# Performance work log

Measured on AMD Instinct MI355X. Metric: run time of the kernel, lower is better.

The kernel has to match this reference:

```python
import jax, jax.numpy as jnp
import numpy as np

N = 100000      # nodes
E = 1600000     # edges (avg degree 16)
IN = 128        # in_channels
HID = 32        # hidden_channels per head
HEADS = 4
OUT = 64        # out_channels
NEG_SLOPE = 0.2 # PyG GATConv default leaky_relu slope


def setup_inputs() -> dict:
    key = jax.random.key(0)
    ks = jax.random.split(key, 12)
    def glorot(k, shape):
        fan = shape[0] + shape[-1]
        s = jnp.sqrt(6.0 / fan)
        return jax.random.uniform(k, shape, jnp.float32, -s, s)
    return {
        "x": jax.random.normal(ks[0], (N, IN), jnp.float32),
        "edge_index": jax.random.randint(ks[1], (2, E), 0, N, dtype=jnp.int64),
        # GATConv layer 1: in=IN, out=HID per head, heads=HEADS, concat=True
        "W1": glorot(ks[2], (IN, HEADS * HID)),
        "a_src1": glorot(ks[3], (HEADS, HID)),
        "a_dst1": glorot(ks[4], (HEADS, HID)),
        "b1": jnp.zeros((HEADS * HID,), jnp.float32),
        # GATConv layer 2: in=HEADS*HID, out=OUT, heads=1, concat=False
        "W2": glorot(ks[5], (HEADS * HID, OUT)),
        "a_src2": glorot(ks[6], (1, OUT)),
        "a_dst2": glorot(ks[7], (1, OUT)),
        "b2": jnp.zeros((OUT,), jnp.float32),
    }


def _gat_layer(x, src, dst, W, a_src, a_dst, bias, num_nodes, concat):
    """PyG-style GATConv (add_self_loops already applied to src/dst).
    x: [N, F_in]; src/dst: [E']; W: [F_in, H*C]; a_*: [H, C]."""
    H, C = a_src.shape
    h = (x @ W).reshape(-1, H, C)                       # [N, H, C]
    # per-node attention scores (avoid gathering full features for logits)
    e_src = (h * a_src[None]).sum(-1)                   # [N, H]
    e_dst = (h * a_dst[None]).sum(-1)                   # [N, H]
    logits = jax.nn.leaky_relu(e_src[src] + e_dst[dst], NEG_SLOPE)  # [E', H]
    # segment softmax over incoming edges of each destination node
    mx = jax.ops.segment_max(logits, dst, num_segments=num_nodes)   # [N, H]
    ex = jnp.exp(logits - mx[dst])                      # [E', H]
    den = jax.ops.segment_sum(ex, dst, num_segments=num_nodes)      # [N, H]
    alpha = ex / (den[dst] + 1e-16)                     # [E', H]
    # weighted message aggregation
    msg = h[src] * alpha[..., None]                     # [E', H, C]
    out = jax.ops.segment_sum(msg, dst, num_segments=num_nodes)     # [N, H, C]
    if concat:
        out = out.reshape(num_nodes, H * C)
    else:
        out = out.mean(axis=1)
    return out + bias


def reference(x, edge_index, W1, a_src1, a_dst1, b1, W2, a_src2, a_dst2, b2):
    n = x.shape[0]
    loops = jnp.arange(n, dtype=edge_index.dtype)
    src = jnp.concatenate([edge_index[0], loops])       # add self-loops (PyG default)
    dst = jnp.concatenate([edge_index[1], loops])
    # dropout layers are identity in eval mode
    h = _gat_layer(x, src, dst, W1, a_src1, a_dst1, b1, n, concat=True)
    h = jax.nn.elu(h)
    out = _gat_layer(h, src, dst, W2, a_src2, a_dst2, b2, n, concat=False)
    return out
```

## Files before the change

### kernel.cpp

```cpp
#include <hip/hip_runtime.h>
#include <cmath>

#define IN_F 128
#define NEG_SLOPE 0.2f
#define SEG 64
#define BSHIFT 7
#define NBMAX 1024
#define CHUNK 2048
#define SLOT 4096
#define LDSTRIDE 136

typedef short bfrag8 __attribute__((ext_vector_type(8)));
typedef float facc4 __attribute__((ext_vector_type(4)));

__device__ __forceinline__ int ldidx(const int* ei, int pos, int is64) {
  return is64 ? ei[2 * pos] : ei[pos];
}
__device__ __forceinline__ unsigned short f2b(float f) {
  unsigned u = __float_as_uint(f);
  u += 0x7fffu + ((u >> 16) & 1u);
  return (unsigned short)(u >> 16);
}
__device__ __forceinline__ float b2f_lo(unsigned u) { return __uint_as_float(u << 16); }
__device__ __forceinline__ float b2f_hi(unsigned u) { return __uint_as_float(u & 0xffff0000u); }
__device__ __forceinline__ float b2f_us(unsigned short us) { return __uint_as_float(((unsigned)us) << 16); }
__device__ __forceinline__ void wave_lds_fence() {
  asm volatile("s_waitcnt lgkmcnt(0)" ::: "memory");
}
__device__ __forceinline__ float leaky(float l) { return fmaxf(l, NEG_SLOPE * l); }

__global__ __launch_bounds__(256) void detect_kernel(const int* __restrict__ ei, int E, int* __restrict__ flag) {
  __shared__ int red[256];
  int acc = 0;
  int limit = E < 4096 ? E : 4096;
  for (int j = threadIdx.x; j < limit; j += 256) acc |= ei[2 * j + 1];
  red[threadIdx.x] = acc;
  __syncthreads();
  for (int s = 128; s > 0; s >>= 1) {
    if ((int)threadIdx.x < s) red[threadIdx.x] |= red[threadIdx.x + s];
    __syncthreads();
  }
  if (threadIdx.x == 0) *flag = (red[0] == 0) ? 1 : 0;
}

__global__ __launch_bounds__(1024) void binit_kernel(int* __restrict__ bcur, int NB) {
  int tid = threadIdx.x;
  if (tid < NB) bcur[tid] = tid * SLOT;
}

__global__ __launch_bounds__(256) void bscatter_kernel(const int* __restrict__ ei, int E, int Etot,
                                                       const int* __restrict__ flag, int NB,
                                                       int* __restrict__ bcur, unsigned* __restrict__ ebuf) {
  __shared__ int hcnt[NBMAX];
  __shared__ int hcur[NBMAX];
  int tid = threadIdx.x;
  int base = blockIdx.x * CHUNK;
  int cnt = Etot - base; if (cnt > CHUNK) cnt = CHUNK;
  int is64 = *flag;
  for (int i = tid; i < NB; i += 256) hcnt[i] = 0;
  __syncthreads();
  for (int i = tid; i < cnt; i += 256) {
    int e = base + i;
    int d = (e < E) ? ldidx(ei, E + e, is64) : (e - E);
    atomicAdd(&hcnt[d >> BSHIFT], 1);
  }
  __syncthreads();
  for (int i = tid; i < NB; i += 256) {
    int c = hcnt[i];
    hcur[i] = c ? atomicAdd(&bcur[i], c) : 0;
  }
  __syncthreads();
  for (int i = tid; i < cnt; i += 256) {
    int e = base + i;
    int s, d;
    if (e < E) { s = ldidx(ei, e, is64); d = ldidx(ei, E + e, is64); }
    else       { s = e - E; d = s; }
    int pos = atomicAdd(&hcur[d >> BSHIFT], 1);
    ebuf[pos] = ((unsigned)s << 7) | ((unsigned)d & 127u);
  }
}

__global__ __launch_bounds__(256) void bcsr_kernel(const int* __restrict__ bcur, const unsigned* __restrict__ ebuf,
                                                   int* __restrict__ rowptr, int* __restrict__ rowdeg,
                                                   int* __restrict__ csr, int N, int NB) {
  __shared__ int cnt[128];
  __shared__ int cur[128];
  __shared__ int w0sum;
  int tid = threadIdx.x;
  int b = blockIdx.x;
  int lo = b * SLOT, hi = bcur[b];
  int node0 = b << BSHIFT;
  int nn = N - node0; if (nn > 128) nn = 128;
  if (tid < 128) cnt[tid] = 0;
  __syncthreads();
  for (int i = lo + tid; i < hi; i += 256) {
    atomicAdd(&cnt[ebuf[i] & 127u], 1);
  }
  __syncthreads();
  int v = 0, incl = 0;
  if (tid < 128) {
    v = cnt[tid];
    incl = v;
    int lane = tid & 63;
    #pragma unroll
    for (int off = 1; off < 64; off <<= 1) { int t = __shfl_up(incl, off); if (lane >= off) incl += t; }
    if (tid == 63) w0sum = incl;
  }
  __syncthreads();
  if (tid < 128) {
    if (tid >= 64) incl += w0sum;
    int excl = incl - v;
    cur[tid] = excl;
    if (tid < nn) {
      rowptr[node0 + tid] = lo + excl;
      rowdeg[node0 + tid] = v;
    }
  }
  __syncthreads();
  for (int i = lo + tid; i < hi; i += 256) {
    unsigned pr = ebuf[i];
    int p = atomicAdd(&cur[pr & 127u], 1);
    csr[lo + p] = (int)(pr >> 7);
  }
}

__global__ __launch_bounds__(256) void gemm1_kernel(
    const float* __restrict__ x, const float* __restrict__ W,
    const float* __restrict__ asr, const float* __restrict__ ads,
    unsigned short* __restrict__ h1b, float* __restrict__ es, float* __restrict__ ed,
    int N) {
  __shared__ short Wt[128 * LDSTRIDE];
  __shared__ short As[64 * LDSTRIDE];
  int tid = threadIdx.x;
  int row0 = blockIdx.x * 64;
  int lane = tid & 63, wv = tid >> 6;
  int m2 = lane & 15, quad = lane >> 4;

  for (int i = tid; i < 128 * 128; i += 256) {
    int k = i >> 7, c = i & 127;
    Wt[c * LDSTRIDE + k] = (short)f2b(W[i]);
  }
  for (int idx = tid; idx < 64 * 16; idx += 256) {
    int r = idx >> 4, ch = idx & 15;
    int n = row0 + r;
    bfrag8 sv;
    if (n < N) {
      float4 v0 = *(const float4*)&x[(size_t)n * 128 + ch * 8];
      float4 v1 = *(const float4*)&x[(size_t)n * 128 + ch * 8 + 4];
      sv[0] = (short)f2b(v0.x); sv[1] = (short)f2b(v0.y);
      sv[2] = (short)f2b(v0.z); sv[3] = (short)f2b(v0.w);
      sv[4] = (short)f2b(v1.x); sv[5] = (short)f2b(v1.y);
      sv[6] = (short)f2b(v1.z); sv[7] = (short)f2b(v1.w);
    } else {
      sv = (bfrag8)0;
    }
    *(bfrag8*)&As[r * LDSTRIDE + ch * 8] = sv;
  }
  __syncthreads();

  facc4 acc[8] = {};
  const short* Abase = &As[(wv * 16 + m2) * LDSTRIDE];
  #pragma unroll
  for (int ks = 0; ks < 4; ++ks) {
    int k = ks * 32 + quad * 8;
    bfrag8 af = *(const bfrag8*)&Abase[k];
    #pragma unroll
    for (int t = 0; t < 8; ++t) {
      bfrag8 bf = *(const bfrag8*)&Wt[(t * 16 + m2) * LDSTRIDE + k];
      acc[t] = __builtin_amdgcn_mfma_f32_16x16x32_bf16(af, bf, acc[t], 0, 0, 0);
    }
  }

  float av[8], bv[8];
  #pragma unroll
  for (int t = 0; t < 8; ++t) {
    int ai = (t >> 1) * 32 + (t & 1) * 16 + m2;
    av[t] = asr[ai]; bv[t] = ads[ai];
  }
  #pragma unroll
  for (int r = 0; r < 4; ++r) {
    int n = row0 + wv * 16 + quad * 4 + r;
    bool valid = (n < N);
    if (valid) {
      #pragma unroll
      for (int t = 0; t < 8; ++t)
        h1b[(size_t)n * 128 + t * 16 + m2] = f2b(acc[t][r]);
    }
    #pragma unroll
    for (int h = 0; h < 4; ++h) {
      float ps = acc[2 * h][r] * av[2 * h] + acc[2 * h + 1][r] * av[2 * h + 1];
      float pd = acc[2 * h][r] * bv[2 * h] + acc[2 * h + 1][r] * bv[2 * h + 1];
      ps += __shfl_xor(ps, 1); ps += __shfl_xor(ps, 2); ps += __shfl_xor(ps, 4); ps += __shfl_xor(ps, 8);
      pd += __shfl_xor(pd, 1); pd += __shfl_xor(pd, 2); pd += __shfl_xor(pd, 4); pd += __shfl_xor(pd, 8);
      if (valid && m2 == 0) {
        es[(size_t)n * 4 + h] = ps;
        ed[(size_t)n * 4 + h] = pd;
      }
    }
  }
}

__global__ __launch_bounds__(256) void gemm2_kernel(
    const unsigned short* __restrict__ xb, const float* __restrict__ W,
    const float* __restrict__ asr, const float* __restrict__ ads,
    unsigned short* __restrict__ h2b, float* __restrict__ es, float* __restrict__ ed,
    int N) {
  __shared__ short Wt[64 * LDSTRIDE];
  __shared__ short As[64 * LDSTRIDE];
  int tid = threadIdx.x;
  int row0 = blockIdx.x * 64;
  int lane = tid & 63, wv = tid >> 6;
  int m2 = lane & 15, quad = lane >> 4;

  for (int i = tid; i < 128 * 64; i += 256) {
    int k = i >> 6, c = i & 63;
    Wt[c * LDSTRIDE + k] = (short)f2b(W[i]);
  }
  for (int idx = tid; idx < 64 * 16; idx += 256) {
    int r = idx >> 4, ch = idx & 15;
    int n = row0 + r;
    uint4 u = (n < N) ? *(const uint4*)&xb[(size_t)n * 128 + ch * 8]
                      : make_uint4(0, 0, 0, 0);
    *(uint4*)&As[r * LDSTRIDE + ch * 8] = u;
  }
  __syncthreads();

  facc4 acc[4] = {};
  const short* Abase = &As[(wv * 16 + m2) * LDSTRIDE];
  #pragma unroll
  for (int ks = 0; ks < 4; ++ks) {
    int k = ks * 32 + quad * 8;
    bfrag8 af = *(const bfrag8*)&Abase[k];
    #pragma unroll
    for (int t = 0; t < 4; ++t) {
      bfrag8 bf = *(const bfrag8*)&Wt[(t * 16 + m2) * LDSTRIDE + k];
      acc[t] = __builtin_amdgcn_mfma_f32_16x16x32_bf16(af, bf, acc[t], 0, 0, 0);
    }
  }

  float av[4], bv[4];
  #pragma unroll
  for (int t = 0; t < 4; ++t) {
    av[t] = asr[t * 16 + m2]; bv[t] = ads[t * 16 + m2];
  }
  #pragma unroll
  for (int r = 0; r < 4; ++r) {
    int n = row0 + wv * 16 + quad * 4 + r;
    bool valid = (n < N);
    if (valid) {
      #pragma unroll
      for (int t = 0; t < 4; ++t)
        h2b[(size_t)n * 64 + t * 16 + m2] = f2b(acc[t][r]);
    }
    float ps = acc[0][r] * av[0] + acc[1][r] * av[1] + acc[2][r] * av[2] + acc[3][r] * av[3];
    float pd = acc[0][r] * bv[0] + acc[1][r] * bv[1] + acc[2][r] * bv[2] + acc[3][r] * bv[3];
    ps += __shfl_xor(ps, 1); ps += __shfl_xor(ps, 2); ps += __shfl_xor(ps, 4); ps += __shfl_xor(ps, 8);
    pd += __shfl_xor(pd, 1); pd += __shfl_xor(pd, 2); pd += __shfl_xor(pd, 4); pd += __shfl_xor(pd, 8);
    if (valid && m2 == 0) { es[n] = ps; ed[n] = pd; }
  }
}

__global__ __launch_bounds__(256) void agg1_kernel(
    const int* __restrict__ rowptr, const int* __restrict__ rowdeg, const int* __restrict__ csr,
    const float* __restrict__ es, const float* __restrict__ ed,
    const unsigned short* __restrict__ h1b, const float* __restrict__ bias1,
    unsigned short* __restrict__ hmidb, int N) {
  __shared__ unsigned short lds_ab[4][4][SEG + 4][4];
  __shared__ int lds_s[4][4][SEG + 4];
  int tid = threadIdx.x;
  int wv = tid >> 6, lane = tid & 63;
  int sub = lane >> 4, sj = lane & 15;
  int nbase = blockIdx.x * 16 + wv * 4;
  int n = nbase + sub;
  bool nvalid = (n < N);
  int start = 0, len = 0;
  if (nvalid) { start = rowptr[n]; len = rowdeg[n]; }
  int lenc = (len <= SEG) ? len : 0;

  float4 edv = nvalid ? ((const float4*)ed)[n] : make_float4(0.f, 0.f, 0.f, 0.f);
  float l[4][4];
  float mx = -1e30f;
  #pragma unroll
  for (int it = 0; it < 4; ++it) {
    int j = sj + it * 16;
    if (j < lenc) {
      int s = csr[start + j];
      lds_s[wv][sub][j] = s;
      float4 ev = ((const float4*)es)[s];
      float l0 = leaky(ev.x + edv.x);
      float l1 = leaky(ev.y + edv.y);
      float l2 = leaky(ev.z + edv.z);
      float l3 = leaky(ev.w + edv.w);
      l[it][0] = l0; l[it][1] = l1; l[it][2] = l2; l[it][3] = l3;
      mx = fmaxf(mx, fmaxf(fmaxf(l0, l1), fmaxf(l2, l3)));
    } else {
      l[it][0] = -1e30f; l[it][1] = -1e30f; l[it][2] = -1e30f; l[it][3] = -1e30f;
    }
  }
  #pragma unroll
  for (int off = 1; off < 16; off <<= 1) mx = fmaxf(mx, __shfl_xor(mx, off));

  float s0 = 0.f, s1 = 0.f, s2 = 0.f, s3 = 0.f;
  #pragma unroll
  for (int it = 0; it < 4; ++it) {
    float p0 = __expf(l[it][0] - mx);
    float p1 = __expf(l[it][1] - mx);
    float p2 = __expf(l[it][2] - mx);
    float p3 = __expf(l[it][3] - mx);
    l[it][0] = p0; l[it][1] = p1; l[it][2] = p2; l[it][3] = p3;
    s0 += p0; s1 += p1; s2 += p2; s3 += p3;
  }
  #pragma unroll
  for (int off = 1; off < 16; off <<= 1) {
    s0 += __shfl_xor(s0, off); s1 += __shfl_xor(s1, off);
    s2 += __shfl_xor(s2, off); s3 += __shfl_xor(s3, off);
  }
  float i0 = __builtin_amdgcn_rcpf(s0 + 1e-16f);
  float i1 = __builtin_amdgcn_rcpf(s1 + 1e-16f);
  float i2 = __builtin_amdgcn_rcpf(s2 + 1e-16f);
  float i3 = __builtin_amdgcn_rcpf(s3 + 1e-16f);
  #pragma unroll
  for (int it = 0; it < 4; ++it) {
    int j = sj + it * 16;
    if (j < lenc) {
      unsigned pk0 = (unsigned)f2b(l[it][0] * i0) | ((unsigned)f2b(l[it][1] * i1) << 16);
      unsigned pk1 = (unsigned)f2b(l[it][2] * i2) | ((unsigned)f2b(l[it][3] * i3) << 16);
      *(unsigned*)&lds_ab[wv][sub][j][0] = pk0;
      *(unsigned*)&lds_ab[wv][sub][j][2] = pk1;
    }
  }
  if (sj == 0) {
    int lenp1 = (lenc + 3) & ~3;
    for (int t = lenc; t < lenp1; ++t) {
      lds_s[wv][sub][t] = 0;
      *(unsigned*)&lds_ab[wv][sub][t][0] = 0u;
      *(unsigned*)&lds_ab[wv][sub][t][2] = 0u;
    }
  }
  wave_lds_fence();

  int fl = lane & 15, eidx = lane >> 4, hd = fl >> 2;
  const uint4* hrow = (const uint4*)h1b;
  #pragma unroll 1
  for (int i = 0; i < 4; ++i) {
    int lenC = __shfl(lenc, i << 4);
    if (lenC == 0) continue;
    int nI = nbase + i;
    const int* sP = &lds_s[wv][i][0];
    const unsigned short* aP = &lds_ab[wv][i][0][hd];
    int lenp = (lenC + 3) & ~3;
    float c0 = 0.f, c1 = 0.f, c2 = 0.f, c3 = 0.f, c4 = 0.f, c5 = 0.f, c6 = 0.f, c7 = 0.f;
    float d0 = 0.f, d1 = 0.f, d2 = 0.f, d3 = 0.f, d4 = 0.f, d5 = 0.f, d6 = 0.f, d7 = 0.f;
    int g = 0;
    for (; g + 8 <= lenp; g += 8) {
      int sA = sP[g + eidx], sB = sP[g + 4 + eidx];
      float wA = b2f_us(aP[(g + eidx) * 4]);
      float wB = b2f_us(aP[(g + 4 + eidx) * 4]);
      uint4 uA = hrow[(size_t)sA * 16 + fl];
      uint4 uB = hrow[(size_t)sB * 16 + fl];
      c0 = fmaf(b2f_lo(uA.x), wA, c0); c1 = fmaf(b2f_hi(uA.x), wA, c1);
      c2 = fmaf(b2f_lo(uA.y), wA, c2); c3 = fmaf(b2f_hi(uA.y), wA, c3);
      c4 = fmaf(b2f_lo(uA.z), wA, c4); c5 = fmaf(b2f_hi(uA.z), wA, c5);
      c6 = fmaf(b2f_lo(uA.w), wA, c6); c7 = fmaf(b2f_hi(uA.w), wA, c7);
      d0 = fmaf(b2f_lo(uB.x), wB, d0); d1 = fmaf(b2f_hi(uB.x), wB, d1);
      d2 = fmaf(b2f_lo(uB.y), wB, d2); d3 = fmaf(b2f_hi(uB.y), wB, d3);
      d4 = fmaf(b2f_lo(uB.z), wB, d4); d5 = fmaf(b2f_hi(uB.z), wB, d5);
      d6 = fmaf(b2f_lo(uB.w), wB, d6); d7 = fmaf(b2f_hi(uB.w), wB, d7);
    }
    if (g < lenp) {
      int sA = sP[g + eidx];
      float wA = b2f_us(aP[(g + eidx) * 4]);
      uint4 uA = hrow[(size_t)sA * 16 + fl];
      c0 = fmaf(b2f_lo(uA.x), wA, c0); c1 = fmaf(b2f_hi(uA.x), wA, c1);
      c2 = fmaf(b2f_lo(uA.y), wA, c2); c3 = fmaf(b2f_hi(uA.y), wA, c3);
      c4 = fmaf(b2f_lo(uA.z), wA, c4); c5 = fmaf(b2f_hi(uA.z), wA, c5);
      c6 = fmaf(b2f_lo(uA.w), wA, c6); c7 = fmaf(b2f_hi(uA.w), wA, c7);
    }
    c0 += d0; c1 += d1; c2 += d2; c3 += d3; c4 += d4; c5 += d5; c6 += d6; c7 += d7;
    c0 += __shfl_xor(c0, 16); c1 += __shfl_xor(c1, 16); c2 += __shfl_xor(c2, 16); c3 += __shfl_xor(c3, 16);
    c4 += __shfl_xor(c4, 16); c5 += __shfl_xor(c5, 16); c6 += __shfl_xor(c6, 16); c7 += __shfl_xor(c7, 16);
    c0 += __shfl_xor(c0, 32); c1 += __shfl_xor(c1, 32); c2 += __shfl_xor(c2, 32); c3 += __shfl_xor(c3, 32);
    c4 += __shfl_xor(c4, 32); c5 += __shfl_xor(c5, 32); c6 += __shfl_xor(c6, 32); c7 += __shfl_xor(c7, 32);
    if (eidx == 0) {
      float4 ba = *(const float4*)&bias1[fl * 8];
      float4 bb = *(const float4*)&bias1[fl * 8 + 4];
      float o0 = c0 + ba.x, o1 = c1 + ba.y, o2 = c2 + ba.z, o3 = c3 + ba.w;
      float o4 = c4 + bb.x, o5 = c5 + bb.y, o6 = c6 + bb.z, o7 = c7 + bb.w;
      o0 = o0 > 0.f ? o0 : expm1f(o0); o1 = o1 > 0.f ? o1 : expm1f(o1);
      o2 = o2 > 0.f ? o2 : expm1f(o2); o3 = o3 > 0.f ? o3 : expm1f(o3);
      o4 = o4 > 0.f ? o4 : expm1f(o4); o5 = o5 > 0.f ? o5 : expm1f(o5);
      o6 = o6 > 0.f ? o6 : expm1f(o6); o7 = o7 > 0.f ? o7 : expm1f(o7);
      uint4 pk;
      pk.x = (unsigned)f2b(o0) | ((unsigned)f2b(o1) << 16);
      pk.y = (unsigned)f2b(o2) | ((unsigned)f2b(o3) << 16);
      pk.z = (unsigned)f2b(o4) | ((unsigned)f2b(o5) << 16);
      pk.w = (unsigned)f2b(o6) | ((unsigned)f2b(o7) << 16);
      ((uint4*)hmidb)[(size_t)nI * 16 + fl] = pk;
    }
  }

  #pragma unroll 1
  for (int i = 0; i < 4; ++i) {
    int lenF = __shfl(len, i << 4);
    if (lenF <= SEG) continue;
    int stF = __shfl(start, i << 4);
    int nI = nbase + i;
    float4 ed4 = ((const float4*)ed)[nI];
    int f = lane * 2, hh = lane >> 4;
    const unsigned* h32 = (const unsigned*)h1b;
    float m0 = -1e30f, m1 = -1e30f, m2 = -1e30f, m3 = -1e30f;
    for (int j = stF + lane; j < stF + lenF; j += 64) {
      int s = csr[j];
      float4 ev = ((const float4*)es)[s];
      m0 = fmaxf(m0, leaky(ev.x + ed4.x)); m1 = fmaxf(m1, leaky(ev.y + ed4.y));
      m2 = fmaxf(m2, leaky(ev.z + ed4.z)); m3 = fmaxf(m3, leaky(ev.w + ed4.w));
    }
    #pragma unroll
    for (int off = 32; off; off >>= 1) {
      m0 = fmaxf(m0, __shfl_xor(m0, off)); m1 = fmaxf(m1, __shfl_xor(m1, off));
      m2 = fmaxf(m2, __shfl_xor(m2, off)); m3 = fmaxf(m3, __shfl_xor(m3, off));
    }
    float t0 = 0.f, t1 = 0.f, t2 = 0.f, t3 = 0.f;
    for (int j = stF + lane; j < stF + lenF; j += 64) {
      int s = csr[j];
      float4 ev = ((const float4*)es)[s];
      t0 += __expf(leaky(ev.x + ed4.x) - m0); t1 += __expf(leaky(ev.y + ed4.y) - m1);
      t2 += __expf(leaky(ev.z + ed4.z) - m2); t3 += __expf(leaky(ev.w + ed4.w) - m3);
    }
    #pragma unroll
    for (int off = 32; off; off >>= 1) {
      t0 += __shfl_xor(t0, off); t1 += __shfl_xor(t1, off);
      t2 += __shfl_xor(t2, off); t3 += __shfl_xor(t3, off);
    }
    float j0 = 1.f / (t0 + 1e-16f), j1 = 1.f / (t1 + 1e-16f);
    float j2 = 1.f / (t2 + 1e-16f), j3 = 1.f / (t3 + 1e-16f);
    float edh = (hh & 2) ? ((hh & 1) ? ed4.w : ed4.z) : ((hh & 1) ? ed4.y : ed4.x);
    float mh  = (hh & 2) ? ((hh & 1) ? m3 : m2) : ((hh & 1) ? m1 : m0);
    float ih  = (hh & 2) ? ((hh & 1) ? j3 : j2) : ((hh & 1) ? j1 : j0);
    float ax = 0.f, ay = 0.f;
    for (int j = stF; j < stF + lenF; ++j) {
      int s = csr[j];
      float lv = leaky(es[(size_t)s * 4 + hh] + edh);
      float a = __expf(lv - mh) * ih;
      unsigned u = h32[(size_t)s * 64 + lane];
      ax = fmaf(b2f_lo(u), a, ax);
      ay = fmaf(b2f_hi(u), a, ay);
    }
    float o0 = ax + bias1[f], o1 = ay + bias1[f + 1];
    o0 = o0 > 0.f ? o0 : expm1f(o0);
    o1 = o1 > 0.f ? o1 : expm1f(o1);
    unsigned packed = (unsigned)f2b(o0) | ((unsigned)f2b(o1) << 16);
    ((unsigned*)hmidb)[(size_t)nI * 64 + lane] = packed;
  }
}

__global__ __launch_bounds__(256) void agg2_kernel(
    const int* __restrict__ rowptr, const int* __restrict__ rowdeg, const int* __restrict__ csr,
    const float* __restrict__ es, const float* __restrict__ ed,
    const unsigned short* __restrict__ h2b, const float* __restrict__ bias2,
    float* __restrict__ out, int N) {
  __shared__ float lds_a[4][4][SEG + 8];
  __shared__ int   lds_s[4][4][SEG + 8];
  int tid = threadIdx.x;
  int wv = tid >> 6, lane = tid & 63;
  int sub = lane >> 4, sj = lane & 15;
  int nbase = blockIdx.x * 16 + wv * 4;
  int n = nbase + sub;
  bool nvalid = (n < N);
  int start = 0, len = 0;
  if (nvalid) { start = rowptr[n]; len = rowdeg[n]; }
  int lenc = (len <= SEG) ? len : 0;

  float edv = nvalid ? ed[n] : 0.f;
  float l[4];
  float mx = -1e30f;
  #pragma unroll
  for (int it = 0; it < 4; ++it) {
    int j = sj + it * 16;
    if (j < lenc) {
      int s = csr[start + j];
      lds_s[wv][sub][j] = s;
      float lv = leaky(es[s] + edv);
      l[it] = lv;
      mx = fmaxf(mx, lv);
    } else {
      l[it] = -1e30f;
    }
  }
  #pragma unroll
  for (int off = 1; off < 16; off <<= 1) mx = fmaxf(mx, __shfl_xor(mx, off));
  float sm = 0.f;
  #pragma unroll
  for (int it = 0; it < 4; ++it) {
    float p = __expf(l[it] - mx);
    l[it] = p;
    sm += p;
  }
  #pragma unroll
  for (int off = 1; off < 16; off <<= 1) sm += __shfl_xor(sm, off);
  float inv = __builtin_amdgcn_rcpf(sm + 1e-16f);
  #pragma unroll
  for (int it = 0; it < 4; ++it) {
    int j = sj + it * 16;
    if (j < lenc) lds_a[wv][sub][j] = l[it] * inv;
  }
  if (sj == 0) {
    int lenp1 = (lenc + 7) & ~7;
    for (int t = lenc; t < lenp1; ++t) {
      lds_s[wv][sub][t] = 0;
      lds_a[wv][sub][t] = 0.f;
    }
  }
  wave_lds_fence();

  int fl = lane & 7, eidx = lane >> 3;
  const uint4* hrow = (const uint4*)h2b;
  #pragma unroll 1
  for (int i = 0; i < 4; ++i) {
    int lenC = __shfl(lenc, i << 4);
    if (lenC == 0) continue;
    int nI = nbase + i;
    const float* aP = &lds_a[wv][i][0];
    const int*   sP = &lds_s[wv][i][0];
    int lenp = (lenC + 7) & ~7;
    float c0 = 0.f, c1 = 0.f, c2 = 0.f, c3 = 0.f, c4 = 0.f, c5 = 0.f, c6 = 0.f, c7 = 0.f;
    for (int g = 0; g < lenp; g += 8) {
      int sA = sP[g + eidx];
      float wA = aP[g + eidx];
      uint4 uA = hrow[(size_t)sA * 8 + fl];
      c0 = fmaf(b2f_lo(uA.x), wA, c0); c1 = fmaf(b2f_hi(uA.x), wA, c1);
      c2 = fmaf(b2f_lo(uA.y), wA, c2); c3 = fmaf(b2f_hi(uA.y), wA, c3);
      c4 = fmaf(b2f_lo(uA.z), wA, c4); c5 = fmaf(b2f_hi(uA.z), wA, c5);
      c6 = fmaf(b2f_lo(uA.w), wA, c6); c7 = fmaf(b2f_hi(uA.w), wA, c7);
    }
    c0 += __shfl_xor(c0, 8);  c1 += __shfl_xor(c1, 8);  c2 += __shfl_xor(c2, 8);  c3 += __shfl_xor(c3, 8);
    c4 += __shfl_xor(c4, 8);  c5 += __shfl_xor(c5, 8);  c6 += __shfl_xor(c6, 8);  c7 += __shfl_xor(c7, 8);
    c0 += __shfl_xor(c0, 16); c1 += __shfl_xor(c1, 16); c2 += __shfl_xor(c2, 16); c3 += __shfl_xor(c3, 16);
    c4 += __shfl_xor(c4, 16); c5 += __shfl_xor(c5, 16); c6 += __shfl_xor(c6, 16); c7 += __shfl_xor(c7, 16);
    c0 += __shfl_xor(c0, 32); c1 += __shfl_xor(c1, 32); c2 += __shfl_xor(c2, 32); c3 += __shfl_xor(c3, 32);
    c4 += __shfl_xor(c4, 32); c5 += __shfl_xor(c5, 32); c6 += __shfl_xor(c6, 32); c7 += __shfl_xor(c7, 32);
    if (eidx == 0) {
      float4 ba = *(const float4*)&bias2[fl * 8];
      float4 bb = *(const float4*)&bias2[fl * 8 + 4];
      ((float4*)out)[(size_t)nI * 16 + fl * 2]     = make_float4(c0 + ba.x, c1 + ba.y, c2 + ba.z, c3 + ba.w);
      ((float4*)out)[(size_t)nI * 16 + fl * 2 + 1] = make_float4(c4 + bb.x, c5 + bb.y, c6 + bb.z, c7 + bb.w);
    }
  }

  #pragma unroll 1
  for (int i = 0; i < 4; ++i) {
    int lenF = __shfl(len, i << 4);
    if (lenF <= SEG) continue;
    int stF = __shfl(start, i << 4);
    int nI = nbase + i;
    float edF = ed[nI];
    float m = -1e30f;
    for (int j = stF + lane; j < stF + lenF; j += 64) {
      m = fmaxf(m, leaky(es[csr[j]] + edF));
    }
    #pragma unroll
    for (int off = 32; off; off >>= 1) m = fmaxf(m, __shfl_xor(m, off));
    float t = 0.f;
    for (int j = stF + lane; j < stF + lenF; j += 64) {
      t += __expf(leaky(es[csr[j]] + edF) - m);
    }
    #pragma unroll
    for (int off = 32; off; off >>= 1) t += __shfl_xor(t, off);
    float iv = 1.f / (t + 1e-16f);
    float acc = 0.f;
    for (int j = stF; j < stF + lenF; ++j) {
      int s = csr[j];
      float a = __expf(leaky(es[s] + edF) - m) * iv;
      float v = __uint_as_float(((unsigned)h2b[(size_t)s * 64 + lane]) << 16);
      acc = fmaf(v, a, acc);
    }
    out[(size_t)nI * 64 + lane] = acc + bias2[lane];
  }
}

extern "C" void kernel_launch(void* const* d_in, const int* in_sizes, int n_in,
                              void* d_out, int out_size, void* d_ws, size_t ws_size,
                              hipStream_t stream) {
  const float* x   = (const float*)d_in[0];
  const int*   ei  = (const int*)d_in[1];
  const float* W1  = (const float*)d_in[2];
  const float* as1 = (const float*)d_in[3];
  const float* ad1 = (const float*)d_in[4];
  const float* b1  = (const float*)d_in[5];
  const float* W2  = (const float*)d_in[6];
  const float* as2 = (const float*)d_in[7];
  const float* ad2 = (const float*)d_in[8];
  const float* b2  = (const float*)d_in[9];
  float* out = (float*)d_out;

  int N = in_sizes[0] / IN_F;
  int E = in_sizes[1] / 2;
  int Etot = E + N;
  int NB = (N + 127) >> BSHIFT;

  char* p = (char*)d_ws;
  auto carve = [&](size_t bytes) -> char* {
    char* r = p;
    p += (bytes + 255) & ~(size_t)255;
    return r;
  };
  int* flag     = (int*)carve(4);
  int* bcur     = (int*)carve((size_t)NBMAX * 4);
  unsigned* ebuf = (unsigned*)carve((size_t)NB * SLOT * 4);
  int* rowptr   = (int*)carve((size_t)(N + 1) * 4);
  int* rowdeg   = (int*)carve((size_t)(N + 1) * 4);
  int* csr      = (int*)carve((size_t)NB * SLOT * 4);
  float* es1    = (float*)carve((size_t)N * 4 * 4);
  float* ed1    = (float*)carve((size_t)N * 4 * 4);
  float* es2    = (float*)carve((size_t)N * 4);
  float* ed2    = (float*)carve((size_t)N * 4);
  unsigned short* h1b   = (unsigned short*)carve((size_t)N * 128 * 2);
  unsigned short* hmidb = (unsigned short*)carve((size_t)N * 128 * 2);
  unsigned short* h2b   = (unsigned short*)carve((size_t)N * 64 * 2);

  int nchunk = (Etot + CHUNK - 1) / CHUNK;
  detect_kernel<<<1, 256, 0, stream>>>(ei, E, flag);
  binit_kernel<<<1, 1024, 0, stream>>>(bcur, NB);
  bscatter_kernel<<<nchunk, 256, 0, stream>>>(ei, E, Etot, flag, NB, bcur, ebuf);
  bcsr_kernel<<<NB, 256, 0, stream>>>(bcur, ebuf, rowptr, rowdeg, csr, N, NB);
  gemm1_kernel<<<(N + 63) / 64, 256, 0, stream>>>(x, W1, as1, ad1, h1b, es1, ed1, N);
  agg1_kernel<<<(N + 15) / 16, 256, 0, stream>>>(rowptr, rowdeg, csr, es1, ed1, h1b, b1, hmidb, N);
  gemm2_kernel<<<(N + 63) / 64, 256, 0, stream>>>(hmidb, W2, as2, ad2, h2b, es2, ed2, N);
  agg2_kernel<<<(N + 15) / 16, 256, 0, stream>>>(rowptr, rowdeg, csr, es2, ed2, h2b, b2, out, N);
}
```

Measured before the change: 338.0 us.

## Unroll agg2 gather loop, store fp32 attention in LDS, use fast ELU

Several unrelated tweaks land together. The agg2 gather loop is unrolled by two with a second set of accumulators, to put more independent loads in flight. agg1 now keeps attention weights as fp32 in a head-major LDS layout instead of packed bf16, which removes the conversions and strided reads. ELU uses __expf(x)-1 instead of expm1f, and CHUNK grows from 2048 to 8192. The trade-off is more LDS use in agg1, higher register pressure, and slightly lower ELU precision near zero.

```diff
diff --git a/kernel.cpp b/kernel.cpp
--- a/kernel.cpp
+++ b/kernel.cpp
@@ -6,7 +6,7 @@
 #define SEG 64
 #define BSHIFT 7
 #define NBMAX 1024
-#define CHUNK 2048
+#define CHUNK 8192
 #define SLOT 4096
 #define LDSTRIDE 136
 
@@ -23,11 +23,11 @@
 }
 __device__ __forceinline__ float b2f_lo(unsigned u) { return __uint_as_float(u << 16); }
 __device__ __forceinline__ float b2f_hi(unsigned u) { return __uint_as_float(u & 0xffff0000u); }
-__device__ __forceinline__ float b2f_us(unsigned short us) { return __uint_as_float(((unsigned)us) << 16); }
 __device__ __forceinline__ void wave_lds_fence() {
   asm volatile("s_waitcnt lgkmcnt(0)" ::: "memory");
 }
 __device__ __forceinline__ float leaky(float l) { return fmaxf(l, NEG_SLOPE * l); }
+__device__ __forceinline__ float elu(float o) { return o > 0.f ? o : __expf(o) - 1.f; }
 
 __global__ __launch_bounds__(256) void detect_kernel(const int* __restrict__ ei, int E, int* __restrict__ flag) {
   __shared__ int red[256];
@@ -265,8 +265,8 @@
     const float* __restrict__ es, const float* __restrict__ ed,
     const unsigned short* __restrict__ h1b, const float* __restrict__ bias1,
     unsigned short* __restrict__ hmidb, int N) {
-  __shared__ unsigned short lds_ab[4][4][SEG + 4][4];
-  __shared__ int lds_s[4][4][SEG + 4];
+  __shared__ float lds_a[4][4][4][SEG + 4];
+  __shared__ int   lds_s[4][4][SEG + 4];
   int tid = threadIdx.x;
   int wv = tid >> 6, lane = tid & 63;
   int sub = lane >> 4, sj = lane & 15;
@@ -323,18 +323,18 @@
   for (int it = 0; it < 4; ++it) {
     int j = sj + it * 16;
     if (j < lenc) {
-      unsigned pk0 = (unsigned)f2b(l[it][0] * i0) | ((unsigned)f2b(l[it][1] * i1) << 16);
-      unsigned pk1 = (unsigned)f2b(l[it][2] * i2) | ((unsigned)f2b(l[it][3] * i3) << 16);
-      *(unsigned*)&lds_ab[wv][sub][j][0] = pk0;
-      *(unsigned*)&lds_ab[wv][sub][j][2] = pk1;
+      lds_a[wv][sub][0][j] = l[it][0] * i0;
+      lds_a[wv][sub][1][j] = l[it][1] * i1;
+      lds_a[wv][sub][2][j] = l[it][2] * i2;
+      lds_a[wv][sub][3][j] = l[it][3] * i3;
     }
   }
   if (sj == 0) {
     int lenp1 = (lenc + 3) & ~3;
     for (int t = lenc; t < lenp1; ++t) {
       lds_s[wv][sub][t] = 0;
-      *(unsigned*)&lds_ab[wv][sub][t][0] = 0u;
-      *(unsigned*)&lds_ab[wv][sub][t][2] = 0u;
+      lds_a[wv][sub][0][t] = 0.f; lds_a[wv][sub][1][t] = 0.f;
+      lds_a[wv][sub][2][t] = 0.f; lds_a[wv][sub][3][t] = 0.f;
     }
   }
   wave_lds_fence();
@@ -347,15 +347,15 @@
     if (lenC == 0) continue;
     int nI = nbase + i;
     const int* sP = &lds_s[wv][i][0];
-    const unsigned short* aP = &lds_ab[wv][i][0][hd];
+    const float* aP = &lds_a[wv][i][hd][0];
     int lenp = (lenC + 3) & ~3;
     float c0 = 0.f, c1 = 0.f, c2 = 0.f, c3 = 0.f, c4 = 0.f, c5 = 0.f, c6 = 0.f, c7 = 0.f;
     float d0 = 0.f, d1 = 0.f, d2 = 0.f, d3 = 0.f, d4 = 0.f, d5 = 0.f, d6 = 0.f, d7 = 0.f;
     int g = 0;
     for (; g + 8 <= lenp; g += 8) {
       int sA = sP[g + eidx], sB = sP[g + 4 + eidx];
-      float wA = b2f_us(aP[(g + eidx) * 4]);
-      float wB = b2f_us(aP[(g + 4 + eidx) * 4]);
+      float wA = aP[g + eidx];
+      float wB = aP[g + 4 + eidx];
       uint4 uA = hrow[(size_t)sA * 16 + fl];
       uint4 uB = hrow[(size_t)sB * 16 + fl];
       c0 = fmaf(b2f_lo(uA.x), wA, c0); c1 = fmaf(b2f_hi(uA.x), wA, c1);
@@ -369,7 +369,7 @@
     }
     if (g < lenp) {
       int sA = sP[g + eidx];
-      float wA = b2f_us(aP[(g + eidx) * 4]);
+      float wA = aP[g + eidx];
       uint4 uA = hrow[(size_t)sA * 16 + fl];
       c0 = fmaf(b2f_lo(uA.x), wA, c0); c1 = fmaf(b2f_hi(uA.x), wA, c1);
       c2 = fmaf(b2f_lo(uA.y), wA, c2); c3 = fmaf(b2f_hi(uA.y), wA, c3);
@@ -384,12 +384,8 @@
     if (eidx == 0) {
       float4 ba = *(const float4*)&bias1[fl * 8];
       float4 bb = *(const float4*)&bias1[fl * 8 + 4];
-      float o0 = c0 + ba.x, o1 = c1 + ba.y, o2 = c2 + ba.z, o3 = c3 + ba.w;
-      float o4 = c4 + bb.x, o5 = c5 + bb.y, o6 = c6 + bb.z, o7 = c7 + bb.w;
-      o0 = o0 > 0.f ? o0 : expm1f(o0); o1 = o1 > 0.f ? o1 : expm1f(o1);
-      o2 = o2 > 0.f ? o2 : expm1f(o2); o3 = o3 > 0.f ? o3 : expm1f(o3);
-      o4 = o4 > 0.f ? o4 : expm1f(o4); o5 = o5 > 0.f ? o5 : expm1f(o5);
-      o6 = o6 > 0.f ? o6 : expm1f(o6); o7 = o7 > 0.f ? o7 : expm1f(o7);
+      float o0 = elu(c0 + ba.x), o1 = elu(c1 + ba.y), o2 = elu(c2 + ba.z), o3 = elu(c3 + ba.w);
+      float o4 = elu(c4 + bb.x), o5 = elu(c5 + bb.y), o6 = elu(c6 + bb.z), o7 = elu(c7 + bb.w);
       uint4 pk;
       pk.x = (unsigned)f2b(o0) | ((unsigned)f2b(o1) << 16);
       pk.y = (unsigned)f2b(o2) | ((unsigned)f2b(o3) << 16);
@@ -446,9 +442,7 @@
       ax = fmaf(b2f_lo(u), a, ax);
       ay = fmaf(b2f_hi(u), a, ay);
     }
-    float o0 = ax + bias1[f], o1 = ay + bias1[f + 1];
-    o0 = o0 > 0.f ? o0 : expm1f(o0);
-    o1 = o1 > 0.f ? o1 : expm1f(o1);
+    float o0 = elu(ax + bias1[f]), o1 = elu(ay + bias1[f + 1]);
     unsigned packed = (unsigned)f2b(o0) | ((unsigned)f2b(o1) << 16);
     ((unsigned*)hmidb)[(size_t)nI * 64 + lane] = packed;
   }
@@ -524,7 +518,23 @@
     const int*   sP = &lds_s[wv][i][0];
     int lenp = (lenC + 7) & ~7;
     float c0 = 0.f, c1 = 0.f, c2 = 0.f, c3 = 0.f, c4 = 0.f, c5 = 0.f, c6 = 0.f, c7 = 0.f;
-    for (int g = 0; g < lenp; g += 8) {
+    float d0 = 0.f, d1 = 0.f, d2 = 0.f, d3 = 0.f, d4 = 0.f, d5 = 0.f, d6 = 0.f, d7 = 0.f;
+    int g = 0;
+    for (; g + 16 <= lenp; g += 16) {
+      int sA = sP[g + eidx],   sB = sP[g + 8 + eidx];
+      float wA = aP[g + eidx], wB = aP[g + 8 + eidx];
+      uint4 uA = hrow[(size_t)sA * 8 + fl];
+      uint4 uB = hrow[(size_t)sB * 8 + fl];
+      c0 = fmaf(b2f_lo(uA.x), wA, c0); c1 = fmaf(b2f_hi(uA.x), wA, c1);
+      c2 = fmaf(b2f_lo(uA.y), wA, c2); c3 = fmaf(b2f_hi(uA.y), wA, c3);
+      c4 = fmaf(b2f_lo(uA.z), wA, c4); c5 = fmaf(b2f_hi(uA.z), wA, c5);
+      c6 = fmaf(b2f_lo(uA.w), wA, c6); c7 = fmaf(b2f_hi(uA.w), wA, c7);
+      d0 = fmaf(b2f_lo(uB.x), wB, d0); d1 = fmaf(b2f_hi(uB.x), wB, d1);
+      d2 = fmaf(b2f_lo(uB.y), wB, d2); d3 = fmaf(b2f_hi(uB.y), wB, d3);
+      d4 = fmaf(b2f_lo(uB.z), wB, d4); d5 = fmaf(b2f_hi(uB.z), wB, d5);
+      d6 = fmaf(b2f_lo(uB.w), wB, d6); d7 = fmaf(b2f_hi(uB.w), wB, d7);
+    }
+    if (g < lenp) {
       int sA = sP[g + eidx];
       float wA = aP[g + eidx];
       uint4 uA = hrow[(size_t)sA * 8 + fl];
@@ -533,6 +543,7 @@
       c4 = fmaf(b2f_lo(uA.z), wA, c4); c5 = fmaf(b2f_hi(uA.z), wA, c5);
       c6 = fmaf(b2f_lo(uA.w), wA, c6); c7 = fmaf(b2f_hi(uA.w), wA, c7);
     }
+    c0 += d0; c1 += d1; c2 += d2; c3 += d3; c4 += d4; c5 += d5; c6 += d6; c7 += d7;
     c0 += __shfl_xor(c0, 8);  c1 += __shfl_xor(c1, 8);  c2 += __shfl_xor(c2, 8);  c3 += __shfl_xor(c3, 8);
     c4 += __shfl_xor(c4, 8);  c5 += __shfl_xor(c5, 8);  c6 += __shfl_xor(c6, 8);  c7 += __shfl_xor(c7, 8);
     c0 += __shfl_xor(c0, 16); c1 += __shfl_xor(c1, 16); c2 += __shfl_xor(c2, 16); c3 += __shfl_xor(c3, 16);
```

Result: no change. 333.2 us (-1.4%).
